# Optimization experiments

Measured on AMD Instinct MI355X. Metric: run time of the kernel, lower is better.

## Reference

```python
import jax, jax.numpy as jnp
import numpy as np

B, C, H, W = 4, 64, 64, 64
INTER, HALF = C // 8, C // 2  # 8, 32


def setup_inputs() -> dict:
    key = jax.random.key(0)
    ks = jax.random.split(key, 10)
    return {
        "x": jax.random.normal(ks[0], (B, C, H, W), jnp.float32),
        "Wf": jax.random.normal(ks[1], (INTER, C), jnp.float32) * 0.1,
        "bf": jax.random.normal(ks[2], (INTER,), jnp.float32) * 0.1,
        "Wg": jax.random.normal(ks[3], (INTER, C), jnp.float32) * 0.1,
        "bg": jax.random.normal(ks[4], (INTER,), jnp.float32) * 0.1,
        "Wh": jax.random.normal(ks[5], (HALF, C), jnp.float32) * 0.1,
        "bh": jax.random.normal(ks[6], (HALF,), jnp.float32) * 0.1,
        "Wv": jax.random.normal(ks[7], (C, HALF), jnp.float32) * 0.1,
        "bv": jax.random.normal(ks[8], (C,), jnp.float32) * 0.1,
        "gamma": jax.random.normal(ks[9], (1,), jnp.float32),
    }


def reference(x, Wf, bf, Wg, bg, Wh, bh, Wv, bv, gamma):
    b, c, h, w = x.shape
    n = h * w
    xf = x.reshape(b, c, n)  # [B, C, N]
    # 1x1 convs are channel matmuls
    f = jnp.einsum('oc,bcn->bno', Wf, xf) + bf            # [B, N, inter] (key, transposed)
    g = jnp.einsum('oc,bcn->bon', Wg, xf) + bg[:, None]   # [B, inter, N] (query)
    hv = jnp.einsum('oc,bcn->bon', Wh, xf) + bh[:, None]  # [B, half, N]  (value)
    # attn[b,i,j] = softmax_j( f[b,i,:] . g[b,:,j] )  (no scaling, as in source)
    attn = jax.nn.softmax(jnp.einsum('bno,bom->bnm', f, g), axis=-1)  # [B, N, N]
    # o[b,c,i] = sum_j hv[b,c,j] * attn[b,i,j]
    o = jnp.einsum('bcm,bnm->bcn', hv, attn)              # [B, half, N]
    o = jnp.einsum('oc,bcn->bon', Wv, o) + bv[:, None]    # [B, C, N]
    return gamma * o.reshape(b, c, h, w) + x
```

## Files before the change

### kernel.cpp

```cpp
#include <hip/hip_runtime.h>
#include <math.h>

#define BB 4
#define CC 64
#define NN 4096
#define IND 8
#define HF 32
#define QBLK 64
#define THREADS 512
#define WAVES 8
#define MBLK 32
#define MCHUNK (NN/WAVES)
#define NBLK (MCHUNK/MBLK)

typedef __attribute__((ext_vector_type(8))) short bf16x8;
typedef __attribute__((ext_vector_type(4))) float f32x4;

static __device__ __forceinline__ unsigned short f2bf(float x) {
    unsigned int u = __float_as_uint(x);
    u = (u + 0x7FFFu + ((u >> 16) & 1u)) >> 16;
    return (unsigned short)u;
}
static __device__ __forceinline__ float bf2f(unsigned short h) {
    return __uint_as_float(((unsigned int)h) << 16);
}
static __device__ __forceinline__ unsigned int pk2(float lo, float hi) {
    __bf16 l = (__bf16)lo, h = (__bf16)hi;
    unsigned short ul = __builtin_bit_cast(unsigned short, l);
    unsigned short uh = __builtin_bit_cast(unsigned short, h);
    return (unsigned int)ul | ((unsigned int)uh << 16);
}
static __device__ __forceinline__ float ex2(float x) {
    return __builtin_amdgcn_exp2f(x);
}


__global__ __launch_bounds__(128) void proj_kernel(
    const float* __restrict__ xsrc,
    const float* __restrict__ Wf, const float* __restrict__ bf,
    const float* __restrict__ Wg, const float* __restrict__ bg,
    const float* __restrict__ Wh, const float* __restrict__ bh,
    unsigned short* __restrict__ fpk,
    unsigned short* __restrict__ gpk,
    unsigned short* __restrict__ vblk)
{
    __shared__ float swT[CC][8];

    int tid = threadIdx.x;
    int bx  = blockIdx.x;
    int og  = bx >> 7;
    int r   = bx & 127;
    int xcd = r & 7;
    int b   = xcd >> 1;
    int blk = ((xcd & 1) << 4) + (r >> 3);
    int n   = blk * 128 + tid;

    const float* W;
    const float* bias;
    if (og == 0)      { W = Wf; bias = bf; }
    else if (og == 1) { W = Wg; bias = bg; }
    else              { W = Wh + (og - 2) * 8 * CC; bias = bh + (og - 2) * 8; }

    {
        float4 wv = *(const float4*)(W + tid * 4);
        int o = (tid * 4) >> 6;
        int c0 = (tid * 4) & 63;
        swT[c0 + 0][o] = wv.x;
        swT[c0 + 1][o] = wv.y;
        swT[c0 + 2][o] = wv.z;
        swT[c0 + 3][o] = wv.w;
    }

    float xv[CC];
    {
        const float* xp = xsrc + (size_t)b * CC * NN + n;
        #pragma unroll
        for (int c = 0; c < CC; c++) xv[c] = xp[(size_t)c * NN];
    }
    #pragma unroll
    for (int c = 0; c < CC; c++) asm volatile("" : "+v"(xv[c]));

    __syncthreads();

    float a[8];
    #pragma unroll
    for (int o = 0; o < 8; o++) a[o] = bias[o];
    #pragma unroll
    for (int c = 0; c < CC; c++) {
        float4 w0 = *(const float4*)&swT[c][0];
        float4 w1 = *(const float4*)&swT[c][4];
        float v = xv[c];
        a[0] += w0.x * v; a[1] += w0.y * v; a[2] += w0.z * v; a[3] += w0.w * v;
        a[4] += w1.x * v; a[5] += w1.y * v; a[6] += w1.z * v; a[7] += w1.w * v;
    }

    const float LOG2E = 1.4426950408889634f;
    size_t base = (size_t)b * NN + n;

    if (og == 0) {
        union { unsigned short s[16]; uint4 q[2]; } fo;
        #pragma unroll
        for (int o = 0; o < 8; o++) {
            unsigned short hi = f2bf(a[o]);
            unsigned short lo = f2bf(a[o] - bf2f(hi));
            fo.s[o] = hi; fo.s[8 + o] = lo;
        }
        uint4* fdst = (uint4*)(fpk + base * 16);
        fdst[0] = fo.q[0]; fdst[1] = fo.q[1];
    } else if (og == 1) {
        union { unsigned short s[16]; uint4 q[2]; } go;
        #pragma unroll
        for (int o = 0; o < 8; o++) {
            float gsc = a[o] * LOG2E;
            unsigned short hi = f2bf(gsc);
            unsigned short lo = f2bf(gsc - bf2f(hi));
            go.s[o] = hi; go.s[8 + o] = lo;
        }
        uint4* gdst = (uint4*)(gpk + base * 16);
        gdst[0] = go.q[0]; gdst[1] = go.q[1];
    } else {
        int m5 = n & 31;
        int code = (m5 & 3) | (((m5 >> 4) & 1) << 2) | (((m5 >> 2) & 3) << 3);
        int mb = (n >> 5);
        int h0 = (og - 2) * 8;
        int hg = h0 >> 4;
        unsigned short* vp = vblk + (size_t)b * (NN/32) * 1024
                           + (size_t)mb * 1024 + hg * 512 + code;
        #pragma unroll
        for (int o = 0; o < 8; o++)
            vp[((h0 + o) & 15) * 32] = f2bf(a[o]);
    }
}

__global__ __launch_bounds__(THREADS, 2) void attn_kernel(
    const unsigned short* __restrict__ fpk,
    const unsigned short* __restrict__ gpk,
    const unsigned short* __restrict__ vblk,
    const float* __restrict__ Wv, const float* __restrict__ bv,
    const float* __restrict__ gamma,
    const float* __restrict__ x, float* __restrict__ out)
{
    __shared__ float sl[WAVES][QBLK][HF + 1];

    int tid  = threadIdx.x;
    int wave = tid >> 6;
    int lane = tid & 63;
    int c15  = lane & 15;
    int g4   = lane >> 4;

    int l  = (blockIdx.x & 7) * 32 + (blockIdx.x >> 3);
    int b  = l >> 6;
    int n0 = (l & 63) * QBLK;

    bf16x8 bq[4];
    #pragma unroll
    for (int qg = 0; qg < 4; qg++)
        bq[qg] = *(const bf16x8*)(fpk
                  + ((size_t)(b * NN + n0 + qg*16 + c15)) * 16 + (g4 & 1) * 8);

    f32x4 zero4 = {0.f, 0.f, 0.f, 0.f};
    f32x4 acc[4][2];
    f32x4 accL[4];
    #pragma unroll
    for (int qg = 0; qg < 4; qg++) {
        acc[qg][0] = zero4; acc[qg][1] = zero4; accL[qg] = zero4;
    }
    const short one_bf = (short)0x3F80;
    const bf16x8 vones = {one_bf, one_bf, one_bf, one_bf,
                          one_bf, one_bf, one_bf, one_bf};

    const unsigned short* gp = gpk  + (size_t)b * NN * 16
                             + ((size_t)(wave * MCHUNK + c15)) * 16 + (g4 >> 1) * 8;
    const unsigned short* vp = vblk + (size_t)b * (NN/32) * 1024
                             + (size_t)(wave * NBLK) * 1024 + c15*32 + g4*8;

#define PREFETCH(tt, ak, vb) do {                                   \
        const unsigned short* g_ = gp + (size_t)(tt) * 512;         \
        const unsigned short* v_ = vp + (size_t)(tt) * 1024;        \
        ak[0] = *(const bf16x8*)(g_);                               \
        ak[1] = *(const bf16x8*)(g_ + 256);                         \
        vb[0] = *(const bf16x8*)(v_);                               \
        vb[1] = *(const bf16x8*)(v_ + 512);                         \
    } while (0)

#define COMPUTE(ak, vb) do {                                        \
        f32x4 sf[4][2];                                             \
        __builtin_amdgcn_s_setprio(1);                              \
        _Pragma("unroll")                                           \
        for (int mg = 0; mg < 2; mg++)                              \
            _Pragma("unroll")                                       \
            for (int qg = 0; qg < 4; qg++)                          \
                sf[qg][mg] = __builtin_amdgcn_mfma_f32_16x16x32_bf16( \
                    ak[mg], bq[qg], zero4, 0, 0, 0);                \
        __builtin_amdgcn_s_setprio(0);                              \
        bf16x8 pa[4];                                               \
        _Pragma("unroll")                                           \
        for (int qg = 0; qg < 4; qg++) {                            \
            float e00 = ex2(sf[qg][0][0]), e01 = ex2(sf[qg][0][1]); \
            float e02 = ex2(sf[qg][0][2]), e03 = ex2(sf[qg][0][3]); \
            float e10 = ex2(sf[qg][1][0]), e11 = ex2(sf[qg][1][1]); \
            float e12 = ex2(sf[qg][1][2]), e13 = ex2(sf[qg][1][3]); \
            union { unsigned int u[4]; bf16x8 v; } pp;              \
            pp.u[0] = pk2(e00, e01); pp.u[1] = pk2(e02, e03);       \
            pp.u[2] = pk2(e10, e11); pp.u[3] = pk2(e12, e13);       \
            pa[qg] = pp.v;                                          \
        }                                                           \
        __builtin_amdgcn_s_setprio(1);                              \
        _Pragma("unroll")                                           \
        for (int qg = 0; qg < 4; qg++) {                            \
            _Pragma("unroll")                                       \
            for (int hg = 0; hg < 2; hg++)                          \
                acc[qg][hg] = __builtin_amdgcn_mfma_f32_16x16x32_bf16( \
                    pa[qg], vb[hg], acc[qg][hg], 0, 0, 0);          \
            accL[qg] = __builtin_amdgcn_mfma_f32_16x16x32_bf16(     \
                    pa[qg], vones, accL[qg], 0, 0, 0);              \
        }                                                           \
        __builtin_amdgcn_s_setprio(0);                              \
    } while (0)

    bf16x8 akA[2], vbA[2], akB[2], vbB[2];
    PREFETCH(0, akA, vbA);

    #pragma unroll 2
    for (int tp = 0; tp < NBLK; tp += 2) {
        PREFETCH(tp + 1, akB, vbB);
        COMPUTE(akA, vbA);
        if (tp + 2 < NBLK) PREFETCH(tp + 2, akA, vbA);
        COMPUTE(akB, vbB);
    }
#undef PREFETCH
#undef COMPUTE

    #pragma unroll
    for (int qg = 0; qg < 4; qg++)
        #pragma unroll
        for (int hg = 0; hg < 2; hg++)
            #pragma unroll
            for (int r = 0; r < 4; r++)
                sl[wave][qg*16 + g4*4 + r][hg*16 + c15] = acc[qg][hg][r];
    if (c15 == 0) {
        #pragma unroll
        for (int qg = 0; qg < 4; qg++)
            #pragma unroll
            for (int r = 0; r < 4; r++)
                sl[wave][qg*16 + g4*4 + r][HF] = accL[qg][r];
    }
    __syncthreads();

    {
        int q = tid & 63;
        for (int col = tid >> 6; col < HF + 1; col += 8) {
            float s = sl[0][q][col];
            #pragma unroll
            for (int w2 = 1; w2 < WAVES; w2++) s += sl[w2][q][col];
            sl[0][q][col] = s;
        }
    }
    __syncthreads();

    int q  = tid & 63;
    int cb = tid >> 6;
    float rL = 1.f / sl[0][q][HF];
    float o_[HF];
    #pragma unroll
    for (int h = 0; h < HF; h++) o_[h] = sl[0][q][h] * rL;
    float gm = gamma[0];
    size_t obase = (size_t)b * CC * NN + n0 + q;
    for (int c = cb*8; c < cb*8 + 8; c++) {
        float v = bv[c];
        #pragma unroll
        for (int h = 0; h < HF; h++) v += Wv[c*HF + h] * o_[h];
        size_t a = obase + (size_t)c * NN;
        out[a] = gm * v + x[a];
    }
}

extern "C" void kernel_launch(void* const* d_in, const int* in_sizes, int n_in,
                              void* d_out, int out_size, void* d_ws, size_t ws_size,
                              hipStream_t stream) {
    const float* x     = (const float*)d_in[0];
    const float* Wf    = (const float*)d_in[1];
    const float* bf    = (const float*)d_in[2];
    const float* Wg    = (const float*)d_in[3];
    const float* bg    = (const float*)d_in[4];
    const float* Wh    = (const float*)d_in[5];
    const float* bh    = (const float*)d_in[6];
    const float* Wv    = (const float*)d_in[7];
    const float* bv    = (const float*)d_in[8];
    const float* gamma = (const float*)d_in[9];
    float* out = (float*)d_out;

    unsigned short* ws   = (unsigned short*)d_ws;
    unsigned short* fpk  = ws;
    unsigned short* gpk  = ws + (size_t)BB*NN*16;
    unsigned short* vblk = ws + (size_t)BB*NN*32;

    proj_kernel<<<(BB*NN/128)*6, 128, 0, stream>>>(x, Wf, bf, Wg, bg, Wh, bh,
                                                   fpk, gpk, vblk);
    attn_kernel<<<BB*(NN/QBLK), THREADS, 0, stream>>>(fpk, gpk, vblk,
                                                      Wv, bv, gamma, x, out);
}
```

Baseline: 28.85 us.

## Fuse projection and attention into one cooperative kernel with grid sync

Merges the projection and attention kernels into a single cooperative launch. Each 512-thread block runs three 128-thread projection sub-blocks (the fourth group idles), then a grid-wide sync, then the attention phase, with shared memory reused across the two phases. The aim is to remove the second launch and the gap between kernels. The cost is a grid sync barrier, cooperative launch overhead, a quarter of threads idle during projection, and occupancy limits on the 256-block grid.

```diff
diff --git a/kernel.cpp b/kernel.cpp
--- a/kernel.cpp
+++ b/kernel.cpp
@@ -1,5 +1,8 @@
 #include <hip/hip_runtime.h>
+#include <hip/hip_cooperative_groups.h>
 #include <math.h>
+
+namespace cg = cooperative_groups;
 
 #define BB 4
 #define CC 64
@@ -35,144 +38,147 @@
 }
 
 
-__global__ __launch_bounds__(128) void proj_kernel(
-    const float* __restrict__ xsrc,
+__global__ __launch_bounds__(THREADS, 2) void fused_kernel(
+    const float* __restrict__ x,
     const float* __restrict__ Wf, const float* __restrict__ bf,
     const float* __restrict__ Wg, const float* __restrict__ bg,
     const float* __restrict__ Wh, const float* __restrict__ bh,
+    const float* __restrict__ Wv, const float* __restrict__ bv,
+    const float* __restrict__ gamma,
     unsigned short* __restrict__ fpk,
     unsigned short* __restrict__ gpk,
-    unsigned short* __restrict__ vblk)
+    unsigned short* __restrict__ vblk,
+    float* __restrict__ out)
 {
-    __shared__ float swT[CC][8];
+    __shared__ float smem[WAVES * QBLK * (HF + 1)];
 
     int tid = threadIdx.x;
-    int bx  = blockIdx.x;
-    int og  = bx >> 7;
-    int r   = bx & 127;
-    int xcd = r & 7;
-    int b   = xcd >> 1;
-    int blk = ((xcd & 1) << 4) + (r >> 3);
-    int n   = blk * 128 + tid;
-
-    const float* W;
-    const float* bias;
-    if (og == 0)      { W = Wf; bias = bf; }
-    else if (og == 1) { W = Wg; bias = bg; }
-    else              { W = Wh + (og - 2) * 8 * CC; bias = bh + (og - 2) * 8; }
 
     {
-        float4 wv = *(const float4*)(W + tid * 4);
-        int o = (tid * 4) >> 6;
-        int c0 = (tid * 4) & 63;
-        swT[c0 + 0][o] = wv.x;
-        swT[c0 + 1][o] = wv.y;
-        swT[c0 + 2][o] = wv.z;
-        swT[c0 + 3][o] = wv.w;
+        int grp = tid >> 7;
+        int lt  = tid & 127;
+        bool active = (grp < 3);
+        int vbx = blockIdx.x * 3 + grp;
+        float* swTg = smem + grp * (CC * 8);
+
+        int og = 0, b = 0, n = 0;
+        const float* W = Wf; const float* bias = bf;
+        if (active) {
+            og = vbx >> 7;
+            int r   = vbx & 127;
+            int xcd = r & 7;
+            b   = xcd >> 1;
+            int blk = ((xcd & 1) << 4) + (r >> 3);
+            n   = blk * 128 + lt;
+            if (og == 0)      { W = Wf; bias = bf; }
+            else if (og == 1) { W = Wg; bias = bg; }
+            else              { W = Wh + (og - 2) * 8 * CC; bias = bh + (og - 2) * 8; }
+        }
+
+        float xv[CC];
+        if (active) {
+            float4 wv = *(const float4*)(W + lt * 4);
+            int o  = (lt * 4) >> 6;
+            int c0 = (lt * 4) & 63;
+            swTg[(c0 + 0) * 8 + o] = wv.x;
+            swTg[(c0 + 1) * 8 + o] = wv.y;
+            swTg[(c0 + 2) * 8 + o] = wv.z;
+            swTg[(c0 + 3) * 8 + o] = wv.w;
+            const float* xp = x + (size_t)b * CC * NN + n;
+            #pragma unroll
+            for (int c = 0; c < CC; c++) xv[c] = xp[(size_t)c * NN];
+            #pragma unroll
+            for (int c = 0; c < CC; c++) asm volatile("" : "+v"(xv[c]));
+        }
+        __syncthreads();
+
+        if (active) {
+            float a[8];
+            #pragma unroll
+            for (int o = 0; o < 8; o++) a[o] = bias[o];
+            #pragma unroll
+            for (int c = 0; c < CC; c++) {
+                float4 w0 = *(const float4*)&swTg[c * 8 + 0];
+                float4 w1 = *(const float4*)&swTg[c * 8 + 4];
+                float v = xv[c];
+                a[0] += w0.x*v; a[1] += w0.y*v; a[2] += w0.z*v; a[3] += w0.w*v;
+                a[4] += w1.x*v; a[5] += w1.y*v; a[6] += w1.z*v; a[7] += w1.w*v;
+            }
+
+            const float LOG2E = 1.4426950408889634f;
+            size_t base = (size_t)b * NN + n;
+
+            if (og == 0) {
+                union { unsigned short s[16]; uint4 q[2]; } fo;
+                #pragma unroll
+                for (int o = 0; o < 8; o++) {
+                    unsigned short hi = f2bf(a[o]);
+                    unsigned short lo = f2bf(a[o] - bf2f(hi));
+                    fo.s[o] = hi; fo.s[8 + o] = lo;
+                }
+                uint4* fdst = (uint4*)(fpk + base * 16);
+                fdst[0] = fo.q[0]; fdst[1] = fo.q[1];
+            } else if (og == 1) {
+                union { unsigned short s[16]; uint4 q[2]; } go;
+                #pragma unroll
+                for (int o = 0; o < 8; o++) {
+                    float gsc = a[o] * LOG2E;
+                    unsigned short hi = f2bf(gsc);
+                    unsigned short lo = f2bf(gsc - bf2f(hi));
+                    go.s[o] = hi; go.s[8 + o] = lo;
+                }
+                uint4* gdst = (uint4*)(gpk + base * 16);
+                gdst[0] = go.q[0]; gdst[1] = go.q[1];
+            } else {
+                int m5 = n & 31;
+                int code = (m5 & 3) | (((m5 >> 4) & 1) << 2) | (((m5 >> 2) & 3) << 3);
+                int mb = (n >> 5);
+                int h0 = (og - 2) * 8;
+                int hg = h0 >> 4;
+                unsigned short* vp = vblk + (size_t)b * (NN/32) * 1024
+                                   + (size_t)mb * 1024 + hg * 512 + code;
+                #pragma unroll
+                for (int o = 0; o < 8; o++)
+                    vp[((h0 + o) & 15) * 32] = f2bf(a[o]);
+            }
+        }
     }
 
-    float xv[CC];
+    cg::this_grid().sync();
+
     {
-        const float* xp = xsrc + (size_t)b * CC * NN + n;
+        float (*sl)[QBLK][HF + 1] = (float (*)[QBLK][HF + 1])smem;
+
+        int wave = tid >> 6;
+        int lane = tid & 63;
+        int c15  = lane & 15;
+        int g4   = lane >> 4;
+
+        int l  = (blockIdx.x & 7) * 32 + (blockIdx.x >> 3);
+        int b  = l >> 6;
+        int n0 = (l & 63) * QBLK;
+
+        bf16x8 bq[4];
         #pragma unroll
-        for (int c = 0; c < CC; c++) xv[c] = xp[(size_t)c * NN];
-    }
-    #pragma unroll
-    for (int c = 0; c < CC; c++) asm volatile("" : "+v"(xv[c]));
-
-    __syncthreads();
-
-    float a[8];
-    #pragma unroll
-    for (int o = 0; o < 8; o++) a[o] = bias[o];
-    #pragma unroll
-    for (int c = 0; c < CC; c++) {
-        float4 w0 = *(const float4*)&swT[c][0];
-        float4 w1 = *(const float4*)&swT[c][4];
-        float v = xv[c];
-        a[0] += w0.x * v; a[1] += w0.y * v; a[2] += w0.z * v; a[3] += w0.w * v;
-        a[4] += w1.x * v; a[5] += w1.y * v; a[6] += w1.z * v; a[7] += w1.w * v;
-    }
-
-    const float LOG2E = 1.4426950408889634f;
-    size_t base = (size_t)b * NN + n;
-
-    if (og == 0) {
-        union { unsigned short s[16]; uint4 q[2]; } fo;
+        for (int qg = 0; qg < 4; qg++)
+            bq[qg] = *(const bf16x8*)(fpk
+                      + ((size_t)(b * NN + n0 + qg*16 + c15)) * 16 + (g4 & 1) * 8);
+
+        f32x4 zero4 = {0.f, 0.f, 0.f, 0.f};
+        f32x4 acc[4][2];
+        f32x4 accL[4];
         #pragma unroll
-        for (int o = 0; o < 8; o++) {
-            unsigned short hi = f2bf(a[o]);
-            unsigned short lo = f2bf(a[o] - bf2f(hi));
-            fo.s[o] = hi; fo.s[8 + o] = lo;
-        }
-        uint4* fdst = (uint4*)(fpk + base * 16);
-        fdst[0] = fo.q[0]; fdst[1] = fo.q[1];
-    } else if (og == 1) {
-        union { unsigned short s[16]; uint4 q[2]; } go;
-        #pragma unroll
-        for (int o = 0; o < 8; o++) {
-            float gsc = a[o] * LOG2E;
-            unsigned short hi = f2bf(gsc);
-            unsigned short lo = f2bf(gsc - bf2f(hi));
-            go.s[o] = hi; go.s[8 + o] = lo;
-        }
-        uint4* gdst = (uint4*)(gpk + base * 16);
-        gdst[0] = go.q[0]; gdst[1] = go.q[1];
-    } else {
-        int m5 = n & 31;
-        int code = (m5 & 3) | (((m5 >> 4) & 1) << 2) | (((m5 >> 2) & 3) << 3);
-        int mb = (n >> 5);
-        int h0 = (og - 2) * 8;
-        int hg = h0 >> 4;
-        unsigned short* vp = vblk + (size_t)b * (NN/32) * 1024
-                           + (size_t)mb * 1024 + hg * 512 + code;
-        #pragma unroll
-        for (int o = 0; o < 8; o++)
-            vp[((h0 + o) & 15) * 32] = f2bf(a[o]);
-    }
-}
-
-__global__ __launch_bounds__(THREADS, 2) void attn_kernel(
-    const unsigned short* __restrict__ fpk,
-    const unsigned short* __restrict__ gpk,
-    const unsigned short* __restrict__ vblk,
-    const float* __restrict__ Wv, const float* __restrict__ bv,
-    const float* __restrict__ gamma,
-    const float* __restrict__ x, float* __restrict__ out)
-{
-    __shared__ float sl[WAVES][QBLK][HF + 1];
-
-    int tid  = threadIdx.x;
-    int wave = tid >> 6;
-    int lane = tid & 63;
-    int c15  = lane & 15;
-    int g4   = lane >> 4;
-
-    int l  = (blockIdx.x & 7) * 32 + (blockIdx.x >> 3);
-    int b  = l >> 6;
-    int n0 = (l & 63) * QBLK;
-
-    bf16x8 bq[4];
-    #pragma unroll
-    for (int qg = 0; qg < 4; qg++)
-        bq[qg] = *(const bf16x8*)(fpk
-                  + ((size_t)(b * NN + n0 + qg*16 + c15)) * 16 + (g4 & 1) * 8);
-
-    f32x4 zero4 = {0.f, 0.f, 0.f, 0.f};
-    f32x4 acc[4][2];
-    f32x4 accL[4];
-    #pragma unroll
-    for (int qg = 0; qg < 4; qg++) {
-        acc[qg][0] = zero4; acc[qg][1] = zero4; accL[qg] = zero4;
-    }
-    const short one_bf = (short)0x3F80;
-    const bf16x8 vones = {one_bf, one_bf, one_bf, one_bf,
-                          one_bf, one_bf, one_bf, one_bf};
-
-    const unsigned short* gp = gpk  + (size_t)b * NN * 16
-                             + ((size_t)(wave * MCHUNK + c15)) * 16 + (g4 >> 1) * 8;
-    const unsigned short* vp = vblk + (size_t)b * (NN/32) * 1024
-                             + (size_t)(wave * NBLK) * 1024 + c15*32 + g4*8;
+        for (int qg = 0; qg < 4; qg++) {
+            acc[qg][0] = zero4; acc[qg][1] = zero4; accL[qg] = zero4;
+        }
+        const short one_bf = (short)0x3F80;
+        const bf16x8 vones = {one_bf, one_bf, one_bf, one_bf,
+                              one_bf, one_bf, one_bf, one_bf};
+
+        const unsigned short* gp = gpk  + (size_t)b * NN * 16
+                                 + ((size_t)(wave * MCHUNK + c15)) * 16 + (g4 >> 1) * 8;
+        const unsigned short* vp = vblk + (size_t)b * (NN/32) * 1024
+                                 + (size_t)(wave * NBLK) * 1024 + c15*32 + g4*8;
 
 #define PREFETCH(tt, ak, vb) do {                                   \
         const unsigned short* g_ = gp + (size_t)(tt) * 512;         \
@@ -218,60 +224,63 @@
         __builtin_amdgcn_s_setprio(0);                              \
     } while (0)
 
-    bf16x8 akA[2], vbA[2], akB[2], vbB[2];
-    PREFETCH(0, akA, vbA);
-
-    #pragma unroll 2
-    for (int tp = 0; tp < NBLK; tp += 2) {
-        PREFETCH(tp + 1, akB, vbB);
-        COMPUTE(akA, vbA);
-        if (tp + 2 < NBLK) PREFETCH(tp + 2, akA, vbA);
-        COMPUTE(akB, vbB);
-    }
+        bf16x8 akA[2], vbA[2], akB[2], vbB[2];
+        PREFETCH(0, akA, vbA);
+
+        #pragma unroll 2
+        for (int tp = 0; tp < NBLK; tp += 2) {
+            PREFETCH(tp + 1, akB, vbB);
+            COMPUTE(akA, vbA);
+            if (tp + 2 < NBLK) PREFETCH(tp + 2, akA, vbA);
+            COMPUTE(akB, vbB);
+        }
 #undef PREFETCH
 #undef COMPUTE
 
-    #pragma unroll
-    for (int qg = 0; qg < 4; qg++)
-        #pragma unroll
-        for (int hg = 0; hg < 2; hg++)
-            #pragma unroll
-            for (int r = 0; r < 4; r++)
-                sl[wave][qg*16 + g4*4 + r][hg*16 + c15] = acc[qg][hg][r];
-    if (c15 == 0) {
+        __syncthreads();
+
         #pragma unroll
         for (int qg = 0; qg < 4; qg++)
             #pragma unroll
-            for (int r = 0; r < 4; r++)
-                sl[wave][qg*16 + g4*4 + r][HF] = accL[qg][r];
-    }
-    __syncthreads();
-
-    {
-        int q = tid & 63;
-        for (int col = tid >> 6; col < HF + 1; col += 8) {
-            float s = sl[0][q][col];
-            #pragma unroll
-            for (int w2 = 1; w2 < WAVES; w2++) s += sl[w2][q][col];
-            sl[0][q][col] = s;
-        }
-    }
-    __syncthreads();
-
-    int q  = tid & 63;
-    int cb = tid >> 6;
-    float rL = 1.f / sl[0][q][HF];
-    float o_[HF];
-    #pragma unroll
-    for (int h = 0; h < HF; h++) o_[h] = sl[0][q][h] * rL;
-    float gm = gamma[0];
-    size_t obase = (size_t)b * CC * NN + n0 + q;
-    for (int c = cb*8; c < cb*8 + 8; c++) {
-        float v = bv[c];
+            for (int hg = 0; hg < 2; hg++)
+                #pragma unroll
+                for (int r = 0; r < 4; r++)
+                    sl[wave][qg*16 + g4*4 + r][hg*16 + c15] = acc[qg][hg][r];
+        if (c15 == 0) {
+            #pragma unroll
+            for (int qg = 0; qg < 4; qg++)
+                #pragma unroll
+                for (int r = 0; r < 4; r++)
+                    sl[wave][qg*16 + g4*4 + r][HF] = accL[qg][r];
+        }
+        __syncthreads();
+
+        {
+            int q = tid & 63;
+            for (int col = tid >> 6; col < HF + 1; col += 8) {
+                float s = sl[0][q][col];
+                #pragma unroll
+                for (int w2 = 1; w2 < WAVES; w2++) s += sl[w2][q][col];
+                sl[0][q][col] = s;
+            }
+        }
+        __syncthreads();
+
+        int q  = tid & 63;
+        int cb = tid >> 6;
+        float rL = 1.f / sl[0][q][HF];
+        float o_[HF];
         #pragma unroll
-        for (int h = 0; h < HF; h++) v += Wv[c*HF + h] * o_[h];
-        size_t a = obase + (size_t)c * NN;
-        out[a] = gm * v + x[a];
+        for (int h = 0; h < HF; h++) o_[h] = sl[0][q][h] * rL;
+        float gm = gamma[0];
+        size_t obase = (size_t)b * CC * NN + n0 + q;
+        for (int c = cb*8; c < cb*8 + 8; c++) {
+            float v = bv[c];
+            #pragma unroll
+            for (int h = 0; h < HF; h++) v += Wv[c*HF + h] * o_[h];
+            size_t a = obase + (size_t)c * NN;
+            out[a] = gm * v + x[a];
+        }
     }
 }
 
@@ -295,8 +304,12 @@
     unsigned short* gpk  = ws + (size_t)BB*NN*16;
     unsigned short* vblk = ws + (size_t)BB*NN*32;
 
-    proj_kernel<<<(BB*NN/128)*6, 128, 0, stream>>>(x, Wf, bf, Wg, bg, Wh, bh,
-                                                   fpk, gpk, vblk);
-    attn_kernel<<<BB*(NN/QBLK), THREADS, 0, stream>>>(fpk, gpk, vblk,
-                                                      Wv, bv, gamma, x, out);
-}
+    void* args[] = {
+        (void*)&x, (void*)&Wf, (void*)&bf, (void*)&Wg, (void*)&bg,
+        (void*)&Wh, (void*)&bh, (void*)&Wv, (void*)&bv, (void*)&gamma,
+        (void*)&fpk, (void*)&gpk, (void*)&vblk, (void*)&out
+    };
+    hipLaunchCooperativeKernel((void*)fused_kernel,
+                               dim3(BB*(NN/QBLK)), dim3(THREADS),
+                               args, 0, stream);
+}
```

Result: slower. 73.01 us (+153.1%).
